# Kernel tuning notes

Hardware: AMD Instinct MI355X
Metric: run time of the kernel (lower is better)

The kernel has to match this reference:

```python
import jax, jax.numpy as jnp
import numpy as np

N_EMBD = 1024
N_HEAD = 16
B, T = 4, 2048

def setup_inputs() -> dict:
    key = jax.random.key(0)
    k1, k2, k3 = jax.random.split(key, 3)
    scale = 0.02
    return {
        "x": jax.random.normal(k1, (B, T, N_EMBD), dtype=jnp.float32),
        "W_qkv": jax.random.normal(k2, (N_EMBD, 3 * N_EMBD), dtype=jnp.float32) * scale,
        "b_qkv": jnp.zeros((3 * N_EMBD,), dtype=jnp.float32),
        "W_proj": jax.random.normal(k3, (N_EMBD, N_EMBD), dtype=jnp.float32) * scale,
        "b_proj": jnp.zeros((N_EMBD,), dtype=jnp.float32),
    }

def reference(x, W_qkv, b_qkv, W_proj, b_proj):
    Bb, Tt, C = x.shape
    hs = C // N_HEAD  # head_size
    qkv = x @ W_qkv + b_qkv                      # [B,T,3C]
    q, k, v = jnp.split(qkv, 3, axis=-1)
    # [B,T,C] -> [B,H,T,hs]
    def to_heads(t):
        return t.reshape(Bb, Tt, N_HEAD, hs).transpose(0, 2, 1, 3)
    q, k, v = to_heads(q), to_heads(k), to_heads(v)
    scores = jnp.einsum('bhqd,bhkd->bhqk', q, k) * (1.0 / np.sqrt(hs))
    causal = jnp.tril(jnp.ones((Tt, Tt), dtype=bool))
    scores = jnp.where(causal, scores, -jnp.inf)
    weights = jax.nn.softmax(scores, axis=-1)    # dropout=0.0 -> identity
    out = jnp.einsum('bhqk,bhkd->bhqd', weights, v)
    out = out.transpose(0, 2, 1, 3).reshape(Bb, Tt, C)
    return out @ W_proj + b_proj
```

## Files before the change

kernel.cpp:

```cpp
#include <hip/hip_runtime.h>
#include <cstdint>

typedef _Float16 f16;
typedef _Float16 f16x4 __attribute__((ext_vector_type(4)));
typedef _Float16 f16x8 __attribute__((ext_vector_type(8)));
typedef float f32x4 __attribute__((ext_vector_type(4)));

constexpr int NB = 4, NT = 2048, NC = 1024, NH = 16, HS = 64;
constexpr int Mtot = NB * NT;
constexpr int BM = 128, BN = 128;

__device__ __forceinline__ void gll16(const f16* g, f16* l) {
  __builtin_amdgcn_global_load_lds(
      (const __attribute__((address_space(1))) unsigned int*)(uintptr_t)g,
      (__attribute__((address_space(3))) unsigned int*)(uintptr_t)l, 16, 0, 0);
}

__global__ __launch_bounds__(256) void convert_x(
    const float* __restrict__ X, f16* __restrict__ Xh)
{
  const size_t i = ((size_t)blockIdx.x * 256 + threadIdx.x) * 8;
  float4 a = *reinterpret_cast<const float4*>(X + i);
  float4 b = *reinterpret_cast<const float4*>(X + i + 4);
  f16x8 o;
  o[0] = (f16)a.x; o[1] = (f16)a.y; o[2] = (f16)a.z; o[3] = (f16)a.w;
  o[4] = (f16)b.x; o[5] = (f16)b.y; o[6] = (f16)b.z; o[7] = (f16)b.w;
  *reinterpret_cast<f16x8*>(Xh + i) = o;
}

__global__ __launch_bounds__(256) void transpose_w(
    const float* __restrict__ Wq, const float* __restrict__ Wp,
    f16* __restrict__ Wqt, f16* __restrict__ Wpt)
{
  __shared__ __align__(16) f16 Ts[64 * 72];
  const int bx = blockIdx.x;
  const float* src; f16* dst; int Ndim, n0;
  if (bx < 48) { src = Wq; dst = Wqt; Ndim = 3 * NC; n0 = bx * 64; }
  else         { src = Wp; dst = Wpt; Ndim = NC;     n0 = (bx - 48) * 64; }
  const int k0 = blockIdx.y * 64;
  const int t = threadIdx.x;
  const int kl = t >> 2, nb = (t & 3) * 16;
#pragma unroll
  for (int i = 0; i < 4; ++i) {
    float4 vv = *reinterpret_cast<const float4*>(
        src + (size_t)(k0 + kl) * Ndim + n0 + nb + 4 * i);
    f16x4 h; h[0] = (f16)vv.x; h[1] = (f16)vv.y; h[2] = (f16)vv.z; h[3] = (f16)vv.w;
    *reinterpret_cast<f16x4*>(&Ts[kl * 72 + nb + 4 * i]) = h;
  }
  __syncthreads();
  const int nl = t >> 2, kb = (t & 3) * 16;
#pragma unroll
  for (int i = 0; i < 2; ++i) {
    f16x8 o;
#pragma unroll
    for (int j = 0; j < 8; ++j) o[j] = Ts[(kb + 8 * i + j) * 72 + nl];
    *reinterpret_cast<f16x8*>(dst + (size_t)(n0 + nl) * NC + k0 + kb + 8 * i) = o;
  }
}

template <int MODE>
__global__ __launch_bounds__(256) void gemm_f16(
    const f16* __restrict__ A, const f16* __restrict__ Bt,
    const float* __restrict__ bias,
    f16* __restrict__ Qh, f16* __restrict__ Kh, f16* __restrict__ Vh,
    float* __restrict__ Out, int ntiles)
{
  __shared__ __align__(16) f16 As[BM * 64];
  __shared__ __align__(16) f16 Bs[BN * 64];
  const int tid = threadIdx.x;
  const int flat = blockIdx.x;
  const int cpx = gridDim.x >> 3;
  const int v = (flat & 7) * cpx + (flat >> 3);
  const int m0 = (v / ntiles) * BM;
  const int n0 = (v % ntiles) * BN;
  const int w = tid >> 6, l = tid & 63;
  const int wr = w >> 1, wc = w & 1;
  const int lr = l & 15, hi = l >> 4;

  f32x4 acc[4][4];
#pragma unroll
  for (int i = 0; i < 4; ++i)
#pragma unroll
    for (int j = 0; j < 4; ++j) acc[i][j] = (f32x4){0.f, 0.f, 0.f, 0.f};

  const int lrow = l >> 3;
  const int lsrc = ((l & 7) ^ lrow) * 8;

  for (int k0 = 0; k0 < NC; k0 += 64) {
    __syncthreads();
#pragma unroll
    for (int i = 0; i < 4; ++i) {
      const int rr = 32 * w + 8 * i;
      gll16(A  + (size_t)(m0 + rr + lrow) * NC + k0 + lsrc, &As[rr * 64]);
      gll16(Bt + (size_t)(n0 + rr + lrow) * NC + k0 + lsrc, &Bs[rr * 64]);
    }
    __syncthreads();
#pragma unroll
    for (int kk = 0; kk < 2; ++kk) {
      f16x8 a[4], b[4];
#pragma unroll
      for (int mi = 0; mi < 4; ++mi) {
        int row = wr * 64 + mi * 16 + lr;
        int idx = (row * 64 + kk * 32 + hi * 8) ^ ((row & 7) << 3);
        a[mi] = *reinterpret_cast<const f16x8*>(&As[idx]);
      }
#pragma unroll
      for (int ni = 0; ni < 4; ++ni) {
        int row = wc * 64 + ni * 16 + lr;
        int idx = (row * 64 + kk * 32 + hi * 8) ^ ((row & 7) << 3);
        b[ni] = *reinterpret_cast<const f16x8*>(&Bs[idx]);
      }
#pragma unroll
      for (int mi = 0; mi < 4; ++mi)
#pragma unroll
        for (int ni = 0; ni < 4; ++ni)
          acc[mi][ni] = __builtin_amdgcn_mfma_f32_16x16x32_f16(
              a[mi], b[ni], acc[mi][ni], 0, 0, 0);
    }
  }

  if (MODE == 0) {
#pragma unroll
    for (int ni = 0; ni < 4; ++ni) {
      int colg = n0 + wc * 64 + ni * 16 + lr;
      int which = colg >> 10;
      int c = colg & (NC - 1);
      int h = c >> 6, d = c & 63;
      float bv = bias[colg];
      if (which == 2) {
#pragma unroll
        for (int mi = 0; mi < 4; ++mi) {
          int rowg = m0 + wr * 64 + mi * 16 + hi * 4;
          int b = rowg >> 11, tt = rowg & (NT - 1);
          int slot = ((tt >> 5) & 1) * 32 + ((tt >> 2) & 3) * 8 + ((tt >> 4) & 1) * 4;
          f16x4 pk;
#pragma unroll
          for (int r = 0; r < 4; ++r) pk[r] = (f16)(acc[mi][ni][r] + bv);
          *reinterpret_cast<f16x4*>(
              &Vh[(size_t)(b * NH + h) * NT * HS + (tt >> 6) * 4096 + d * 64 + slot]) = pk;
        }
      } else {
        f16* dst = (which == 0) ? Qh : Kh;
#pragma unroll
        for (int mi = 0; mi < 4; ++mi) {
#pragma unroll
          for (int r = 0; r < 4; ++r) {
            int rowg = m0 + wr * 64 + mi * 16 + hi * 4 + r;
            int b = rowg >> 11, t = rowg & (NT - 1);
            dst[(((size_t)(b * NH + h) * NT) + t) * HS + d] =
                (f16)(acc[mi][ni][r] + bv);
          }
        }
      }
    }
  } else {
#pragma unroll
    for (int ni = 0; ni < 4; ++ni) {
      int colg = n0 + wc * 64 + ni * 16 + lr;
      float bv = bias[colg];
#pragma unroll
      for (int mi = 0; mi < 4; ++mi) {
#pragma unroll
        for (int r = 0; r < 4; ++r) {
          int rowg = m0 + wr * 64 + mi * 16 + hi * 4 + r;
          Out[(size_t)rowg * NC + colg] = acc[mi][ni][r] + bv;
        }
      }
    }
  }
}

__global__ __launch_bounds__(128, 2) void flash_attn(
    const f16* __restrict__ Qh, const f16* __restrict__ Kh,
    const f16* __restrict__ Vh, f16* __restrict__ att)
{
  __shared__ __align__(16) f16 Ks[2][64 * 64];
  __shared__ __align__(16) f16 Vt[2][64 * 64];

  const int tid = threadIdx.x;
  const int w = tid >> 6, l = tid & 63;
  const int lr = l & 15, g = l >> 4;

  const int flat = blockIdx.x;
  const int v = (flat & 7) * 128 + (flat >> 3);
  const int pairi = v & 15;
  const int bh = v >> 4;

  const f16* Qb = Qh + (size_t)bh * NT * HS;
  const f16* Kb = Kh + (size_t)bh * NT * HS;
  const f16* Vb = Vh + (size_t)bh * NT * HS;
  const int ob = bh >> 4, oh = bh & (NH - 1);

  const int srow = tid >> 1;
  const int scol = (tid & 1) * 32;
  const int vs = ((srow + (srow >> 3)) & 7) << 3;

  f16x8 kpre[4], vpre[4];
#pragma unroll
  for (int ii = 0; ii < 4; ++ii) {
    kpre[ii] = *reinterpret_cast<const f16x8*>(Kb + (size_t)srow * HS + scol + 8 * ii);
    vpre[ii] = *reinterpret_cast<const f16x8*>(Vb + (size_t)srow * HS + scol + 8 * ii);
  }

  for (int seg = 0; seg < 2; ++seg) {
    const int qt = (seg == 0) ? pairi : 31 - pairi;
    const int qbase = qt * 64 + w * 32;
    const int jtmax = qt;

    f16x8 qB[2][2];
#pragma unroll
    for (int mt = 0; mt < 2; ++mt)
#pragma unroll
      for (int ds = 0; ds < 2; ++ds) {
        f16x8 t = *reinterpret_cast<const f16x8*>(
            Qb + (size_t)(qbase + 16 * mt + lr) * HS + 32 * ds + 8 * g);
#pragma unroll
        for (int j = 0; j < 8; ++j) t[j] = t[j] * (f16)0.18033688f;
        qB[mt][ds] = t;
      }

    f32x4 Ot[2][4];
    float m_run[2], l_run[2];
#pragma unroll
    for (int mt = 0; mt < 2; ++mt) {
#pragma unroll
      for (int dt = 0; dt < 4; ++dt) Ot[mt][dt] = (f32x4){0.f, 0.f, 0.f, 0.f};
      m_run[mt] = -INFINITY; l_run[mt] = 0.f;
    }

    for (int jt = 0; jt <= jtmax; ++jt) {
      const int cur = jt & 1;
#pragma unroll
      for (int ii = 0; ii < 4; ++ii) {
        int c0 = scol + 8 * ii;
        *reinterpret_cast<f16x8*>(&Ks[cur][srow * 64 + (c0 ^ ((srow & 7) << 3))]) = kpre[ii];
        *reinterpret_cast<f16x8*>(&Vt[cur][srow * 64 + (c0 ^ vs)]) = vpre[ii];
      }
      const bool more = (jt < jtmax) || (seg == 0);
      if (more) {
        const int nj = (jt < jtmax) ? jt + 1 : 0;
#pragma unroll
        for (int ii = 0; ii < 4; ++ii) {
          kpre[ii] = *reinterpret_cast<const f16x8*>(
              Kb + (size_t)(nj * 64 + srow) * HS + scol + 8 * ii);
          vpre[ii] = *reinterpret_cast<const f16x8*>(
              Vb + (size_t)(nj * 64 + srow) * HS + scol + 8 * ii);
        }
      }
      __syncthreads();

      const bool needMask = (jt * 64 + 63) > qbase;

      f16x8 aK[4][2];
#pragma unroll
      for (int kt2 = 0; kt2 < 4; ++kt2) {
        int row = 16 * kt2 + lr;
#pragma unroll
        for (int ds = 0; ds < 2; ++ds)
          aK[kt2][ds] = *reinterpret_cast<const f16x8*>(
              &Ks[cur][row * 64 + ((32 * ds + 8 * g) ^ ((row & 7) << 3))]);
      }

      f16x8 pB[2][2];

#pragma unroll
      for (int mt = 0; mt < 2; ++mt) {
        f32x4 St[4];
#pragma unroll
        for (int kt2 = 0; kt2 < 4; ++kt2) St[kt2] = (f32x4){0.f, 0.f, 0.f, 0.f};
        __builtin_amdgcn_s_setprio(1);
#pragma unroll
        for (int kt2 = 0; kt2 < 4; ++kt2)
#pragma unroll
          for (int ds = 0; ds < 2; ++ds)
            St[kt2] = __builtin_amdgcn_mfma_f32_16x16x32_f16(
                aK[kt2][ds], qB[mt][ds], St[kt2], 0, 0, 0);
        __builtin_amdgcn_s_setprio(0);

        const int qg = qbase + 16 * mt + lr;
        if (needMask) {
#pragma unroll
          for (int kt2 = 0; kt2 < 4; ++kt2)
#pragma unroll
            for (int r = 0; r < 4; ++r)
              if ((jt * 64 + 16 * kt2 + 4 * g + r) > qg) St[kt2][r] = -INFINITY;
        }
        float pm = -INFINITY;
#pragma unroll
        for (int kt2 = 0; kt2 < 4; ++kt2)
#pragma unroll
          for (int r = 0; r < 4; ++r) pm = fmaxf(pm, St[kt2][r]);
        pm = fmaxf(pm, __shfl_xor(pm, 16));
        pm = fmaxf(pm, __shfl_xor(pm, 32));
        float mo = m_run[mt];
        if (!__all(pm <= mo + 8.0f)) {
          float mn = fmaxf(mo, pm);
          float al = exp2f(mo - mn);
          l_run[mt] *= al;
#pragma unroll
          for (int dt = 0; dt < 4; ++dt)
#pragma unroll
            for (int r = 0; r < 4; ++r) Ot[mt][dt][r] *= al;
          m_run[mt] = mn;
          mo = mn;
        }
        float ts = 0.f;
#pragma unroll
        for (int kt2 = 0; kt2 < 4; ++kt2) {
#pragma unroll
          for (int r = 0; r < 4; ++r) {
            float pp = exp2f(St[kt2][r] - mo);
            ts += pp;
            pB[mt][kt2 >> 1][(kt2 & 1) * 4 + r] = (f16)pp;
          }
        }
        ts += __shfl_xor(ts, 16);
        ts += __shfl_xor(ts, 32);
        l_run[mt] += ts;
      }

      __builtin_amdgcn_s_setprio(1);
#pragma unroll
      for (int kt = 0; kt < 2; ++kt)
#pragma unroll
        for (int dt = 0; dt < 4; ++dt) {
          int d = 16 * dt + lr;
          int s = (d + (d >> 3)) & 7;
          f16x8 vA = *reinterpret_cast<const f16x8*>(
              &Vt[cur][d * 64 + ((32 * kt + 8 * g) ^ (s << 3))]);
#pragma unroll
          for (int mt = 0; mt < 2; ++mt)
            Ot[mt][dt] = __builtin_amdgcn_mfma_f32_16x16x32_f16(
                vA, pB[mt][kt], Ot[mt][dt], 0, 0, 0);
        }
      __builtin_amdgcn_s_setprio(0);
    }

    __syncthreads();
    f16* scr = &Ks[0][0] + w * 2048;
#pragma unroll
    for (int mt = 0; mt < 2; ++mt) {
      float inv = 1.f / l_run[mt];
      int q = 16 * mt + lr;
#pragma unroll
      for (int dt = 0; dt < 4; ++dt) {
        f16x4 ok;
#pragma unroll
        for (int r = 0; r < 4; ++r) ok[r] = (f16)(Ot[mt][dt][r] * inv);
        *reinterpret_cast<f16x4*>(
            &scr[q * 64 + ((16 * dt + 4 * g) ^ ((q & 7) << 3))]) = ok;
      }
    }
    const int orow = l >> 1;
    const int ocol = (l & 1) * 32;
#pragma unroll
    for (int i = 0; i < 4; ++i) {
      f16x8 ov = *reinterpret_cast<const f16x8*>(
          &scr[orow * 64 + ((ocol + i * 8) ^ ((orow & 7) << 3))]);
      *reinterpret_cast<f16x8*>(
          &att[((size_t)(ob * NT + qbase + orow)) * NC + oh * HS + ocol + i * 8]) = ov;
    }
    __syncthreads();
  }
}

extern "C" void kernel_launch(void* const* d_in, const int* in_sizes, int n_in,
                              void* d_out, int out_size, void* d_ws, size_t ws_size,
                              hipStream_t stream)
{
  (void)in_sizes; (void)n_in; (void)out_size; (void)ws_size;
  const float* x     = (const float*)d_in[0];
  const float* Wqkv  = (const float*)d_in[1];
  const float* bqkv  = (const float*)d_in[2];
  const float* Wproj = (const float*)d_in[3];
  const float* bproj = (const float*)d_in[4];
  float* out = (float*)d_out;

  const size_t HE = (size_t)NB * NH * NT * HS;
  f16* Qh  = (f16*)d_ws;
  f16* Kh  = Qh + HE;
  f16* Vh  = Kh + HE;
  f16* XA  = Vh + HE;
  f16* Wqt = XA + HE;
  f16* Wpt = Wqt + (size_t)3 * NC * NC;

  convert_x<<<dim3(Mtot * NC / (256 * 8)), 256, 0, stream>>>(x, XA);
  transpose_w<<<dim3(64, 16), 256, 0, stream>>>(Wqkv, Wproj, Wqt, Wpt);
  gemm_f16<0><<<dim3(64 * 24), 256, 0, stream>>>(XA, Wqt, bqkv, Qh, Kh, Vh, nullptr, 24);
  flash_attn<<<dim3(1024), 128, 0, stream>>>(Qh, Kh, Vh, XA);
  gemm_f16<1><<<dim3(64 * 8), 256, 0, stream>>>(XA, Wpt, bproj, nullptr, nullptr, nullptr, out, 8);
}
```

Measured before the change: 187.5 us.

## Stream K via async global-to-LDS loads, read V from global, one q-tile per block

The attention kernel no longer pairs two query tiles per block. It launches one block per query tile, with the longest causal tiles scheduled first. K tiles are double-buffered in LDS using global_load_lds direct copies, which replaces the register-staged prefetch. V fragments are loaded straight from global memory into MFMA operand registers, which removes the V LDS buffer and its stores. This cuts LDS traffic and register staging, but V global-load latency now sits inside each iteration and relies on correct vmcnt waits before the barrier.

```diff
diff --git a/kernel.cpp b/kernel.cpp
--- a/kernel.cpp
+++ b/kernel.cpp
@@ -175,192 +175,179 @@
     const f16* __restrict__ Vh, f16* __restrict__ att)
 {
   __shared__ __align__(16) f16 Ks[2][64 * 64];
-  __shared__ __align__(16) f16 Vt[2][64 * 64];
 
   const int tid = threadIdx.x;
   const int w = tid >> 6, l = tid & 63;
   const int lr = l & 15, g = l >> 4;
 
   const int flat = blockIdx.x;
-  const int v = (flat & 7) * 128 + (flat >> 3);
-  const int pairi = v & 15;
-  const int bh = v >> 4;
+  const int v = (flat & 7) * 256 + (flat >> 3);
+  const int qt = 31 - (v & 31);
+  const int bh = v >> 5;
 
   const f16* Qb = Qh + (size_t)bh * NT * HS;
   const f16* Kb = Kh + (size_t)bh * NT * HS;
   const f16* Vb = Vh + (size_t)bh * NT * HS;
   const int ob = bh >> 4, oh = bh & (NH - 1);
 
-  const int srow = tid >> 1;
-  const int scol = (tid & 1) * 32;
-  const int vs = ((srow + (srow >> 3)) & 7) << 3;
-
-  f16x8 kpre[4], vpre[4];
-#pragma unroll
-  for (int ii = 0; ii < 4; ++ii) {
-    kpre[ii] = *reinterpret_cast<const f16x8*>(Kb + (size_t)srow * HS + scol + 8 * ii);
-    vpre[ii] = *reinterpret_cast<const f16x8*>(Vb + (size_t)srow * HS + scol + 8 * ii);
-  }
-
-  for (int seg = 0; seg < 2; ++seg) {
-    const int qt = (seg == 0) ? pairi : 31 - pairi;
-    const int qbase = qt * 64 + w * 32;
-    const int jtmax = qt;
-
-    f16x8 qB[2][2];
-#pragma unroll
-    for (int mt = 0; mt < 2; ++mt)
-#pragma unroll
-      for (int ds = 0; ds < 2; ++ds) {
-        f16x8 t = *reinterpret_cast<const f16x8*>(
-            Qb + (size_t)(qbase + 16 * mt + lr) * HS + 32 * ds + 8 * g);
-#pragma unroll
-        for (int j = 0; j < 8; ++j) t[j] = t[j] * (f16)0.18033688f;
-        qB[mt][ds] = t;
-      }
-
-    f32x4 Ot[2][4];
-    float m_run[2], l_run[2];
+  const int qbase = qt * 64 + w * 32;
+  const int jtmax = qt;
+
+  const int lrow = l >> 3;
+  const int lsrc = ((l & 7) ^ lrow) * 8;
+
+#pragma unroll
+  for (int i = 0; i < 8; ++i)
+    gll16(Kb + (size_t)(8 * i + lrow) * HS + lsrc, &Ks[0][i * 512]);
+
+  f16x8 qB[2][2];
+#pragma unroll
+  for (int mt = 0; mt < 2; ++mt)
+#pragma unroll
+    for (int ds = 0; ds < 2; ++ds) {
+      f16x8 t = *reinterpret_cast<const f16x8*>(
+          Qb + (size_t)(qbase + 16 * mt + lr) * HS + 32 * ds + 8 * g);
+#pragma unroll
+      for (int j = 0; j < 8; ++j) t[j] = t[j] * (f16)0.18033688f;
+      qB[mt][ds] = t;
+    }
+
+  f32x4 Ot[2][4];
+  float m_run[2], l_run[2];
+#pragma unroll
+  for (int mt = 0; mt < 2; ++mt) {
+#pragma unroll
+    for (int dt = 0; dt < 4; ++dt) Ot[mt][dt] = (f32x4){0.f, 0.f, 0.f, 0.f};
+    m_run[mt] = -INFINITY; l_run[mt] = 0.f;
+  }
+
+  __syncthreads();
+
+  for (int jt = 0; jt <= jtmax; ++jt) {
+    const int cur = jt & 1;
+
+    f16x8 vA[2][4];
+#pragma unroll
+    for (int kt = 0; kt < 2; ++kt)
+#pragma unroll
+      for (int dt = 0; dt < 4; ++dt)
+        vA[kt][dt] = *reinterpret_cast<const f16x8*>(
+            Vb + (size_t)jt * 4096 + (16 * dt + lr) * 64 + 32 * kt + 8 * g);
+
+    if (jt < jtmax) {
+#pragma unroll
+      for (int i = 0; i < 8; ++i)
+        gll16(Kb + (size_t)((jt + 1) * 64 + 8 * i + lrow) * HS + lsrc,
+              &Ks[cur ^ 1][i * 512]);
+    }
+
+    const bool needMask = (jt * 64 + 63) > qbase;
+
+    f16x8 aK[4][2];
+#pragma unroll
+    for (int kt2 = 0; kt2 < 4; ++kt2) {
+      int row = 16 * kt2 + lr;
+#pragma unroll
+      for (int ds = 0; ds < 2; ++ds)
+        aK[kt2][ds] = *reinterpret_cast<const f16x8*>(
+            &Ks[cur][row * 64 + ((32 * ds + 8 * g) ^ ((row & 7) << 3))]);
+    }
+
+    f16x8 pB[2][2];
+
 #pragma unroll
     for (int mt = 0; mt < 2; ++mt) {
-#pragma unroll
-      for (int dt = 0; dt < 4; ++dt) Ot[mt][dt] = (f32x4){0.f, 0.f, 0.f, 0.f};
-      m_run[mt] = -INFINITY; l_run[mt] = 0.f;
-    }
-
-    for (int jt = 0; jt <= jtmax; ++jt) {
-      const int cur = jt & 1;
-#pragma unroll
-      for (int ii = 0; ii < 4; ++ii) {
-        int c0 = scol + 8 * ii;
-        *reinterpret_cast<f16x8*>(&Ks[cur][srow * 64 + (c0 ^ ((srow & 7) << 3))]) = kpre[ii];
-        *reinterpret_cast<f16x8*>(&Vt[cur][srow * 64 + (c0 ^ vs)]) = vpre[ii];
-      }
-      const bool more = (jt < jtmax) || (seg == 0);
-      if (more) {
-        const int nj = (jt < jtmax) ? jt + 1 : 0;
-#pragma unroll
-        for (int ii = 0; ii < 4; ++ii) {
-          kpre[ii] = *reinterpret_cast<const f16x8*>(
-              Kb + (size_t)(nj * 64 + srow) * HS + scol + 8 * ii);
-          vpre[ii] = *reinterpret_cast<const f16x8*>(
-              Vb + (size_t)(nj * 64 + srow) * HS + scol + 8 * ii);
+      f32x4 St[4];
+#pragma unroll
+      for (int kt2 = 0; kt2 < 4; ++kt2) St[kt2] = (f32x4){0.f, 0.f, 0.f, 0.f};
+      __builtin_amdgcn_s_setprio(1);
+#pragma unroll
+      for (int kt2 = 0; kt2 < 4; ++kt2)
+#pragma unroll
+        for (int ds = 0; ds < 2; ++ds)
+          St[kt2] = __builtin_amdgcn_mfma_f32_16x16x32_f16(
+              aK[kt2][ds], qB[mt][ds], St[kt2], 0, 0, 0);
+      __builtin_amdgcn_s_setprio(0);
+
+      const int qg = qbase + 16 * mt + lr;
+      if (needMask) {
+#pragma unroll
+        for (int kt2 = 0; kt2 < 4; ++kt2)
+#pragma unroll
+          for (int r = 0; r < 4; ++r)
+            if ((jt * 64 + 16 * kt2 + 4 * g + r) > qg) St[kt2][r] = -INFINITY;
+      }
+      float pm = -INFINITY;
+#pragma unroll
+      for (int kt2 = 0; kt2 < 4; ++kt2)
+#pragma unroll
+        for (int r = 0; r < 4; ++r) pm = fmaxf(pm, St[kt2][r]);
+      pm = fmaxf(pm, __shfl_xor(pm, 16));
+      pm = fmaxf(pm, __shfl_xor(pm, 32));
+      float mo = m_run[mt];
+      if (!__all(pm <= mo + 8.0f)) {
+        float mn = fmaxf(mo, pm);
+        float al = exp2f(mo - mn);
+        l_run[mt] *= al;
+#pragma unroll
+        for (int dt = 0; dt < 4; ++dt)
+#pragma unroll
+          for (int r = 0; r < 4; ++r) Ot[mt][dt][r] *= al;
+        m_run[mt] = mn;
+        mo = mn;
+      }
+      float ts = 0.f;
+#pragma unroll
+      for (int kt2 = 0; kt2 < 4; ++kt2) {
+#pragma unroll
+        for (int r = 0; r < 4; ++r) {
+          float pp = exp2f(St[kt2][r] - mo);
+          ts += pp;
+          pB[mt][kt2 >> 1][(kt2 & 1) * 4 + r] = (f16)pp;
         }
       }
-      __syncthreads();
-
-      const bool needMask = (jt * 64 + 63) > qbase;
-
-      f16x8 aK[4][2];
-#pragma unroll
-      for (int kt2 = 0; kt2 < 4; ++kt2) {
-        int row = 16 * kt2 + lr;
-#pragma unroll
-        for (int ds = 0; ds < 2; ++ds)
-          aK[kt2][ds] = *reinterpret_cast<const f16x8*>(
-              &Ks[cur][row * 64 + ((32 * ds + 8 * g) ^ ((row & 7) << 3))]);
-      }
-
-      f16x8 pB[2][2];
-
-#pragma unroll
-      for (int mt = 0; mt < 2; ++mt) {
-        f32x4 St[4];
-#pragma unroll
-        for (int kt2 = 0; kt2 < 4; ++kt2) St[kt2] = (f32x4){0.f, 0.f, 0.f, 0.f};
-        __builtin_amdgcn_s_setprio(1);
-#pragma unroll
-        for (int kt2 = 0; kt2 < 4; ++kt2)
-#pragma unroll
-          for (int ds = 0; ds < 2; ++ds)
-            St[kt2] = __builtin_amdgcn_mfma_f32_16x16x32_f16(
-                aK[kt2][ds], qB[mt][ds], St[kt2], 0, 0, 0);
-        __builtin_amdgcn_s_setprio(0);
-
-        const int qg = qbase + 16 * mt + lr;
-        if (needMask) {
-#pragma unroll
-          for (int kt2 = 0; kt2 < 4; ++kt2)
-#pragma unroll
-            for (int r = 0; r < 4; ++r)
-              if ((jt * 64 + 16 * kt2 + 4 * g + r) > qg) St[kt2][r] = -INFINITY;
-        }
-        float pm = -INFINITY;
-#pragma unroll
-        for (int kt2 = 0; kt2 < 4; ++kt2)
-#pragma unroll
-          for (int r = 0; r < 4; ++r) pm = fmaxf(pm, St[kt2][r]);
-        pm = fmaxf(pm, __shfl_xor(pm, 16));
-        pm = fmaxf(pm, __shfl_xor(pm, 32));
-        float mo = m_run[mt];
-        if (!__all(pm <= mo + 8.0f)) {
-          float mn = fmaxf(mo, pm);
-          float al = exp2f(mo - mn);
-          l_run[mt] *= al;
-#pragma unroll
-          for (int dt = 0; dt < 4; ++dt)
-#pragma unroll
-            for (int r = 0; r < 4; ++r) Ot[mt][dt][r] *= al;
-          m_run[mt] = mn;
-          mo = mn;
-        }
-        float ts = 0.f;
-#pragma unroll
-        for (int kt2 = 0; kt2 < 4; ++kt2) {
-#pragma unroll
-          for (int r = 0; r < 4; ++r) {
-            float pp = exp2f(St[kt2][r] - mo);
-            ts += pp;
-            pB[mt][kt2 >> 1][(kt2 & 1) * 4 + r] = (f16)pp;
-          }
-        }
-        ts += __shfl_xor(ts, 16);
-        ts += __shfl_xor(ts, 32);
-        l_run[mt] += ts;
-      }
-
-      __builtin_amdgcn_s_setprio(1);
-#pragma unroll
-      for (int kt = 0; kt < 2; ++kt)
-#pragma unroll
-        for (int dt = 0; dt < 4; ++dt) {
-          int d = 16 * dt + lr;
-          int s = (d + (d >> 3)) & 7;
-          f16x8 vA = *reinterpret_cast<const f16x8*>(
-              &Vt[cur][d * 64 + ((32 * kt + 8 * g) ^ (s << 3))]);
-#pragma unroll
-          for (int mt = 0; mt < 2; ++mt)
-            Ot[mt][dt] = __builtin_amdgcn_mfma_f32_16x16x32_f16(
-                vA, pB[mt][kt], Ot[mt][dt], 0, 0, 0);
-        }
-      __builtin_amdgcn_s_setprio(0);
-    }
+      ts += __shfl_xor(ts, 16);
+      ts += __shfl_xor(ts, 32);
+      l_run[mt] += ts;
+    }
+
+    __builtin_amdgcn_s_setprio(1);
+#pragma unroll
+    for (int kt = 0; kt < 2; ++kt)
+#pragma unroll
+      for (int dt = 0; dt < 4; ++dt) {
+#pragma unroll
+        for (int mt = 0; mt < 2; ++mt)
+          Ot[mt][dt] = __builtin_amdgcn_mfma_f32_16x16x32_f16(
+              vA[kt][dt], pB[mt][kt], Ot[mt][dt], 0, 0, 0);
+      }
+    __builtin_amdgcn_s_setprio(0);
 
     __syncthreads();
-    f16* scr = &Ks[0][0] + w * 2048;
-#pragma unroll
-    for (int mt = 0; mt < 2; ++mt) {
-      float inv = 1.f / l_run[mt];
-      int q = 16 * mt + lr;
-#pragma unroll
-      for (int dt = 0; dt < 4; ++dt) {
-        f16x4 ok;
-#pragma unroll
-        for (int r = 0; r < 4; ++r) ok[r] = (f16)(Ot[mt][dt][r] * inv);
-        *reinterpret_cast<f16x4*>(
-            &scr[q * 64 + ((16 * dt + 4 * g) ^ ((q & 7) << 3))]) = ok;
-      }
-    }
-    const int orow = l >> 1;
-    const int ocol = (l & 1) * 32;
-#pragma unroll
-    for (int i = 0; i < 4; ++i) {
-      f16x8 ov = *reinterpret_cast<const f16x8*>(
-          &scr[orow * 64 + ((ocol + i * 8) ^ ((orow & 7) << 3))]);
-      *reinterpret_cast<f16x8*>(
-          &att[((size_t)(ob * NT + qbase + orow)) * NC + oh * HS + ocol + i * 8]) = ov;
-    }
-    __syncthreads();
+  }
+
+  f16* scr = &Ks[0][0] + w * 2048;
+#pragma unroll
+  for (int mt = 0; mt < 2; ++mt) {
+    float inv = 1.f / l_run[mt];
+    int q = 16 * mt + lr;
+#pragma unroll
+    for (int dt = 0; dt < 4; ++dt) {
+      f16x4 ok;
+#pragma unroll
+      for (int r = 0; r < 4; ++r) ok[r] = (f16)(Ot[mt][dt][r] * inv);
+      *reinterpret_cast<f16x4*>(
+          &scr[q * 64 + ((16 * dt + 4 * g) ^ ((q & 7) << 3))]) = ok;
+    }
+  }
+  const int orow = l >> 1;
+  const int ocol = (l & 1) * 32;
+#pragma unroll
+  for (int i = 0; i < 4; ++i) {
+    f16x8 ov = *reinterpret_cast<const f16x8*>(
+        &scr[orow * 64 + ((ocol + i * 8) ^ ((orow & 7) << 3))]);
+    *reinterpret_cast<f16x8*>(
+        &att[((size_t)(ob * NT + qbase + orow)) * NC + oh * HS + ocol + i * 8]) = ov;
   }
 }
 
@@ -387,6 +374,6 @@
   convert_x<<<dim3(Mtot * NC / (256 * 8)), 256, 0, stream>>>(x, XA);
   transpose_w<<<dim3(64, 16), 256, 0, stream>>>(Wqkv, Wproj, Wqt, Wpt);
   gemm_f16<0><<<dim3(64 * 24), 256, 0, stream>>>(XA, Wqt, bqkv, Qh, Kh, Vh, nullptr, 24);
-  flash_attn<<<dim3(1024), 128, 0, stream>>>(Qh, Kh, Vh, XA);
+  flash_attn<<<dim3(2048), 128, 0, stream>>>(Qh, Kh, Vh, XA);
   gemm_f16<1><<<dim3(64 * 8), 256, 0, stream>>>(XA, Wpt, bproj, nullptr, nullptr, nullptr, out, 8);
 }
```

After: 229.4 us. +22.3%, slower.
